# Performance work log

Measured on AMD Instinct MI355X. Metric: run time of the kernel, lower is better.

## Reference

```python
import jax, jax.numpy as jnp
import numpy as np


def setup_inputs() -> dict:
    key = jax.random.key(0)
    ks = jax.random.split(key, 18)
    B, T, L, C = 16, 512, 50, 7
    H = 512
    s = 0.05
    inp = {
        "phone_data": jax.random.normal(ks[0], (B, T, L, C), jnp.float32),
        "h0": jax.random.normal(ks[1], (B, H), jnp.float32),
        "conv1_w": jax.random.normal(ks[2], (128, 7, 11), jnp.float32) * s,
        "conv1_b": jax.random.normal(ks[3], (128,), jnp.float32) * s,
        "conv2_w": jax.random.normal(ks[4], (256, 128, 9), jnp.float32) * s,
        "conv2_b": jax.random.normal(ks[5], (256,), jnp.float32) * s,
        "fc1_w": jax.random.normal(ks[6], (1024, 1536), jnp.float32) * s,
        "fc1_b": jax.random.normal(ks[7], (1024,), jnp.float32) * s,
        "fc2_w": jax.random.normal(ks[8], (512, 1024), jnp.float32) * s,
        "fc2_b": jax.random.normal(ks[9], (512,), jnp.float32) * s,
        "gru_wih": jax.random.normal(ks[10], (3 * H, H), jnp.float32) * s,
        "gru_whh": jax.random.normal(ks[11], (3 * H, H), jnp.float32) * s,
        "gru_bih": jax.random.normal(ks[12], (3 * H,), jnp.float32) * s,
        "gru_bhh": jax.random.normal(ks[13], (3 * H,), jnp.float32) * s,
        "fc3_w": jax.random.normal(ks[14], (1, H), jnp.float32) * s,
        "fc3_b": jax.random.normal(ks[15], (1,), jnp.float32) * s,
    }
    return inp


def reference(phone_data, h0, conv1_w, conv1_b, conv2_w, conv2_b,
              fc1_w, fc1_b, fc2_w, fc2_b,
              gru_wih, gru_whh, gru_bih, gru_bhh, fc3_w, fc3_b):
    B, T, L, C = phone_data.shape
    N = B * T
    # ---- batched CNN + FC feature extractor (independent per frame) ----
    x = phone_data.reshape(N, L, C).transpose(0, 2, 1)  # [N, 7, 50]
    y = jax.lax.conv_general_dilated(
        x, conv1_w, (1,), 'VALID',
        dimension_numbers=('NCH', 'OIH', 'NCH')) + conv1_b[None, :, None]  # [N,128,40]
    y = y.reshape(N, 128, 20, 2).max(-1)  # maxpool k=2,s=2 -> [N,128,20]
    y = jax.lax.conv_general_dilated(
        y, conv2_w, (1,), 'VALID',
        dimension_numbers=('NCH', 'OIH', 'NCH')) + conv2_b[None, :, None]  # [N,256,12]
    y = y.reshape(N, 256, 6, 2).max(-1)  # [N,256,6]
    feat = y.reshape(N, 1536)            # Flatten(0): channel-major, matches torch
    feat = feat @ fc1_w.T + fc1_b        # [N,1024]
    feat = feat @ fc2_w.T + fc2_b        # [N,512]
    feat = feat.reshape(B, T, 512)

    # ---- sequential GRUCell recurrence (PyTorch GRUCell math) ----
    def cell(h, x_t):
        gi = x_t @ gru_wih.T + gru_bih   # [B, 3H]
        gh = h @ gru_whh.T + gru_bhh     # [B, 3H]
        ir, iz, in_ = jnp.split(gi, 3, axis=-1)
        hr, hz, hn = jnp.split(gh, 3, axis=-1)
        r = jax.nn.sigmoid(ir + hr)
        z = jax.nn.sigmoid(iz + hz)
        n = jnp.tanh(in_ + r * hn)
        h_new = (1 - z) * n + z * h
        # original code calls hx.detach() every step
        h_new = jax.lax.stop_gradient(h_new)
        return h_new, h_new

    _, hs = jax.lax.scan(cell, h0, feat.transpose(1, 0, 2))  # hs: [T,B,512]
    out = hs @ fc3_w.T + fc3_b  # [T,B,1]
    return out.transpose(1, 0, 2)  # [B,T,1]
```

## Files before the change

### kernel.cpp

```cpp
#include <hip/hip_runtime.h>
#include <hip/hip_bf16.h>
#include <math.h>
#include <stdint.h>

typedef __attribute__((ext_vector_type(8))) short short8;
typedef __attribute__((ext_vector_type(4))) float f32x4;
typedef __attribute__((ext_vector_type(4))) unsigned int uint4v;

#define T_ 512

__device__ __forceinline__ unsigned short bf16rn(float f) {
  union { float f; unsigned u; } x; x.f = f;
  unsigned r = x.u + 0x7FFF + ((x.u >> 16) & 1);
  return (unsigned short)(r >> 16);
}

__device__ __forceinline__ void gload16(const void* gsrc, void* ldst) {
  __builtin_amdgcn_global_load_lds(
      (const __attribute__((address_space(1))) unsigned int*)gsrc,
      (__attribute__((address_space(3))) unsigned int*)ldst, 16, 0, 0);
}

__device__ __forceinline__ void wg_barrier() {
  __builtin_amdgcn_sched_barrier(0);
  asm volatile("s_waitcnt lgkmcnt(0)" ::: "memory");
  __builtin_amdgcn_sched_barrier(0);
  __builtin_amdgcn_s_barrier();
  __builtin_amdgcn_sched_barrier(0);
}

__global__ __launch_bounds__(256) void conv1_kernel(
    const float* __restrict__ phone, const float* __restrict__ w1,
    const float* __restrict__ b1, ushort* __restrict__ out1b) {
  __shared__ float ws[128 * 77];
  __shared__ float bs[128];
  __shared__ float xs[8][7][52];
  const int tid = threadIdx.x;
  const int n0 = blockIdx.x * 8;
  for (int idx = tid; idx < 9856; idx += 256) ws[idx] = w1[idx];
  if (tid < 128) bs[tid] = b1[tid];
  for (int idx = tid; idx < 2800; idx += 256) {
    int fi = idx / 350, r = idx - fi * 350;
    int ll = r / 7, c = r - ll * 7;
    xs[fi][c][ll] = phone[(size_t)(n0 + fi) * 350 + r];
  }
  __syncthreads();

  const int o = tid >> 1, ph = tid & 1;
  const float* wo = ws + o * 77;
  const float bb = bs[o];
  for (int fi = 0; fi < 8; ++fi) {
    float acc0[10], acc1[10];
#pragma unroll
    for (int q = 0; q < 10; ++q) { acc0[q] = 0.f; acc1[q] = 0.f; }
    for (int i = 0; i < 7; ++i) {
      float wr[11];
#pragma unroll
      for (int k = 0; k < 11; ++k) wr[k] = wo[i * 11 + k];
#pragma unroll
      for (int q = 0; q < 10; ++q) {
        int p = ph * 10 + q;
        int base = 2 * p;
        float xv[12];
#pragma unroll
        for (int j = 0; j < 12; ++j) xv[j] = xs[fi][i][base + j];
        float s0 = 0.f, s1 = 0.f;
#pragma unroll
        for (int k = 0; k < 11; ++k) {
          s0 += xv[k] * wr[k];
          s1 += xv[k + 1] * wr[k];
        }
        acc0[q] += s0;
        acc1[q] += s1;
      }
    }
#pragma unroll
    for (int q = 0; q < 10; ++q) {
      int p = ph * 10 + q;
      out1b[((size_t)(n0 + fi) * 128 + o) * 20 + p] =
          bf16rn(fmaxf(acc0[q], acc1[q]) + bb);
    }
  }
}

__global__ __launch_bounds__(256) void f32_to_bf16_multi(
    const float* __restrict__ s0, ushort* __restrict__ d0,
    const float* __restrict__ s1, ushort* __restrict__ d1,
    const float* __restrict__ s2, ushort* __restrict__ d2,
    const float* __restrict__ s3, ushort* __restrict__ d3) {
  const int n0 = 73728, n1 = 393216, n2 = 131072, n3 = 196608;
  int i = blockIdx.x * 256 + threadIdx.x;
  const float* s; ushort* d; int off;
  if (i < n0) { s = s0; d = d0; off = i; }
  else if (i < n0 + n1) { s = s1; d = d1; off = i - n0; }
  else if (i < n0 + n1 + n2) { s = s2; d = d2; off = i - n0 - n1; }
  else if (i < n0 + n1 + n2 + n3) { s = s3; d = d3; off = i - n0 - n1 - n2; }
  else return;
  float4 v = ((const float4*)s)[off];
  ushort4 o;
  o.x = bf16rn(v.x); o.y = bf16rn(v.y); o.z = bf16rn(v.z); o.w = bf16rn(v.w);
  ((ushort4*)d)[off] = o;
}

__global__ __launch_bounds__(256) void stage_h0(
    const float* __restrict__ h0, unsigned long long* __restrict__ hxt) {
  const int tid = threadIdx.x;
#pragma unroll
  for (int k = 0; k < 16; ++k) {
    int idx = tid + k * 256;
    int g = idx >> 11, rem = idx & 2047;
    int s = rem >> 7, w_i = rem & 127;
    int b8 = (w_i >> 2) & 7, fqk = w_i >> 5, p2 = w_i & 3;
    int b = g * 8 + b8;
    int D = s * 32 + fqk * 8 + p2 * 2;
    float2 h2 = *(const float2*)(h0 + (size_t)b * 512 + D);
    unsigned pk = (unsigned)bf16rn(h2.x) | ((unsigned)bf16rn(h2.y) << 16);
    hxt[8192 + (size_t)g * 4096 + s * 128 + w_i] = (unsigned long long)pk;
  }
}

template <int AM, int EM>
__global__ __launch_bounds__(256) void gemm_bf16(
    const ushort* __restrict__ A, const ushort* __restrict__ W,
    const float* __restrict__ bias, void* __restrict__ Cout,
    int K, int lda, int ldc) {
  __shared__ ushort As[128 * 64];
  __shared__ ushort Bs[128 * 64];
  __shared__ ushort tbl[1152];
  const int tid = threadIdx.x;
  const int l = tid & 63, wv = tid >> 6;
  const int wr = wv >> 1, wc = wv & 1;
  const int fr = l & 15, fq = l >> 4;
  const int bm0 = blockIdx.x * 128, bn0 = blockIdx.y * 128;

  if (AM == 1) {
    for (int idx = tid; idx < 1152; idx += 256) {
      int i2 = idx / 9, kp = idx - i2 * 9;
      tbl[idx] = (ushort)(i2 * 20 + kp);
    }
    __syncthreads();
  }

  f32x4 acc[4][4];
#pragma unroll
  for (int mi = 0; mi < 4; ++mi)
#pragma unroll
    for (int ni = 0; ni < 4; ++ni) acc[mi][ni] = (f32x4)0.f;

  const int pr8 = l >> 3;
  const int pc = l & 7;
  const int nkt = K >> 6;
  for (int kt = 0; kt < nkt; ++kt) {
    const int k0 = kt << 6;
#pragma unroll
    for (int i = 0; i < 4; ++i) {
      int q = wv * 4 + i;
      int prow = q * 8 + pr8;
      int lc = pc ^ (prow & 7);
      gload16(W + (size_t)(bn0 + prow) * K + k0 + lc * 8, &Bs[q * 512]);
    }
    if (AM == 0) {
#pragma unroll
      for (int i = 0; i < 4; ++i) {
        int q = wv * 4 + i;
        int prow = q * 8 + pr8;
        int lc = pc ^ (prow & 7);
        gload16(A + (size_t)(bm0 + prow) * lda + k0 + lc * 8, &As[q * 512]);
      }
    } else {
#pragma unroll
      for (int q = 0; q < 16; ++q) {
        int idx = tid + q * 256;
        int row = idx >> 5, c0 = (idx & 31) * 2;
        int m = bm0 + row;
        int n = m / 12, pos = m - n * 12;
        int kk = k0 + c0;
        const ushort* an = A + (size_t)n * 2560 + pos;
        uint e0 = an[tbl[kk]];
        uint e1 = an[tbl[kk + 1]];
        *(uint*)&As[row * 64 + (((c0 >> 3) ^ (row & 7)) << 3) + (c0 & 7)] =
            e0 | (e1 << 16);
      }
    }
    __syncthreads();
#pragma unroll
    for (int ks = 0; ks < 2; ++ks) {
      short8 af[4], bfr[4];
#pragma unroll
      for (int mi = 0; mi < 4; ++mi) {
        int row = wr * 64 + mi * 16 + fr;
        af[mi] = *(const short8*)&As[row * 64 + (((ks * 4 + fq) ^ (row & 7)) << 3)];
      }
#pragma unroll
      for (int ni = 0; ni < 4; ++ni) {
        int row = wc * 64 + ni * 16 + fr;
        bfr[ni] = *(const short8*)&Bs[row * 64 + (((ks * 4 + fq) ^ (row & 7)) << 3)];
      }
#pragma unroll
      for (int mi = 0; mi < 4; ++mi)
#pragma unroll
        for (int ni = 0; ni < 4; ++ni)
          acc[mi][ni] = __builtin_amdgcn_mfma_f32_16x16x32_bf16(
              af[mi], bfr[ni], acc[mi][ni], 0, 0, 0);
    }
    __syncthreads();
  }

#pragma unroll
  for (int ni = 0; ni < 4; ++ni) {
    int col = bn0 + wc * 64 + ni * 16 + fr;
    float bv = bias[col];
#pragma unroll
    for (int mi = 0; mi < 4; ++mi) {
      int mbase = bm0 + wr * 64 + mi * 16 + fq * 4;
      if (EM == 0) {
        ushort* C = (ushort*)Cout;
#pragma unroll
        for (int j = 0; j < 4; ++j)
          C[(size_t)(mbase + j) * ldc + col] = bf16rn(acc[mi][ni][j] + bv);
      } else if (EM == 1) {
        ushort* C = (ushort*)Cout;
#pragma unroll
        for (int j = 0; j < 4; j += 2) {
          int m = mbase + j;
          int n = m / 12, pos = m - n * 12;
          float v = fmaxf(acc[mi][ni][j], acc[mi][ni][j + 1]) + bv;
          C[(size_t)n * 1536 + col * 6 + (pos >> 1)] = bf16rn(v);
        }
      } else {
        float* C = (float*)Cout;
#pragma unroll
        for (int j = 0; j < 4; ++j) {
          int m = mbase + j;
          int b = m >> 9, tt = m & 511;
          C[((size_t)tt * 16 + b) * 1536 + col] = acc[mi][ni][j] + bv;
        }
      }
    }
  }
}

__global__ __launch_bounds__(384) void gru_persistent(
    const float* __restrict__ h0, const float* __restrict__ gi,
    const float* __restrict__ whh, const float* __restrict__ bhh,
    float* __restrict__ hsbuf, unsigned long long* __restrict__ hxt) {
  __shared__ float gh_lds[12 * 256];
  __shared__ unsigned afl[16 * 64 * 4];
  const int tid = threadIdx.x;
  const int g = blockIdx.x & 7, wp = blockIdx.x >> 3;
  if (g >= 2) return;
  const int l = tid & 63, v = tid >> 6;
  const int fr = l & 15, fq = l >> 4;
  unsigned long long* hxl = hxt + (size_t)g * 4096;
  unsigned long long* hxm = hxt + 8192 + (size_t)g * 4096;

  const int b8 = tid >> 5, jp = tid & 31, jl = jp * 2;
  const bool gthr = (tid < 256);
  const int pt = tid - 256;

  int s_w = 0, w_w = 0;
  if (gthr) {
    s_w = wp * 2 + (jl >> 5);
    w_w = (((jl & 31) >> 3) * 8 + b8) * 4 + (jp & 3);
    *(volatile unsigned long long*)(hxl + s_w * 128 + w_w) = 0ull;
    *(volatile unsigned long long*)(hxl + 2048 + s_w * 128 + w_w) = 0ull;
  }

  const int t0 = 2 * v, t1 = 2 * v + 1;
  const int o0 = (t0 >> 2) * 512 + wp * 64 + (t0 & 3) * 16 + fr;
  const int o1 = (t1 >> 2) * 512 + wp * 64 + (t1 & 3) * 16 + fr;
  short8 bf0[16], bf1[16];
#pragma unroll
  for (int s = 0; s < 16; ++s) {
    const float* wp0 = whh + (size_t)o0 * 512 + s * 32 + fq * 8;
    const float* wp1 = whh + (size_t)o1 * 512 + s * 32 + fq * 8;
    float4 a0 = *(const float4*)wp0, a1 = *(const float4*)(wp0 + 4);
    float4 c0 = *(const float4*)wp1, c1 = *(const float4*)(wp1 + 4);
    short8 x, y;
    x[0] = (short)bf16rn(a0.x); x[1] = (short)bf16rn(a0.y);
    x[2] = (short)bf16rn(a0.z); x[3] = (short)bf16rn(a0.w);
    x[4] = (short)bf16rn(a1.x); x[5] = (short)bf16rn(a1.y);
    x[6] = (short)bf16rn(a1.z); x[7] = (short)bf16rn(a1.w);
    y[0] = (short)bf16rn(c0.x); y[1] = (short)bf16rn(c0.y);
    y[2] = (short)bf16rn(c0.z); y[3] = (short)bf16rn(c0.w);
    y[4] = (short)bf16rn(c1.x); y[5] = (short)bf16rn(c1.y);
    y[6] = (short)bf16rn(c1.z); y[7] = (short)bf16rn(c1.w);
    bf0[s] = x; bf1[s] = y;
  }
  const float bo0 = bhh[o0], bo1 = bhh[o1];

  const int bglob = g * 8 + b8;
  const int jglob = wp * 64 + jl;
  float hA = 0.f, hB = 0.f;
  float giC0 = 0.f, giC1 = 0.f, giC2 = 0.f, giC3 = 0.f, giC4 = 0.f, giC5 = 0.f;
  float giN0 = 0.f, giN1 = 0.f, giN2 = 0.f, giN3 = 0.f, giN4 = 0.f, giN5 = 0.f;
  if (gthr) {
    float2 h2 = *(const float2*)(h0 + (size_t)bglob * 512 + jglob);
    hA = h2.x; hB = h2.y;
    const float* g0 = gi + (size_t)bglob * 1536 + jglob;
    float2 r0 = *(const float2*)(g0);
    float2 r1 = *(const float2*)(g0 + 512);
    float2 r2 = *(const float2*)(g0 + 1024);
    giC0 = r0.x; giC3 = r0.y; giC1 = r1.x; giC4 = r1.y; giC2 = r2.x; giC5 = r2.y;
    const float* g1 = gi + (size_t)(16 + bglob) * 1536 + jglob;
    float2 s0 = *(const float2*)(g1);
    float2 s1 = *(const float2*)(g1 + 512);
    float2 s2 = *(const float2*)(g1 + 1024);
    giN0 = s0.x; giN3 = s0.y; giN1 = s1.x; giN4 = s1.y; giN2 = s2.x; giN5 = s2.y;
  }

  bool useMir = false;
  if (!gthr) {
    const int ps = pt >> 3;
    const int pw0 = (pt & 7) * 2;
    const unsigned long long* base = hxm + ps * 128;
    uint4v r[8];
    for (;;) {
#pragma unroll
      for (int m = 0; m < 8; ++m)
        asm volatile("global_load_dwordx4 %0, %1, off sc0 sc1"
                     : "=v"(r[m]) : "v"(base + pw0 + m * 16));
      asm volatile("s_waitcnt vmcnt(0)" ::: "memory");
      __builtin_amdgcn_sched_barrier(0);
      bool ok = true;
#pragma unroll
      for (int m = 0; m < 8; ++m)
        ok = ok & (r[m].y == 0u) & (r[m].w == 0u);
      if (ok) break;
    }
#pragma unroll
    for (int m = 0; m < 8; ++m) {
      int w_i = pw0 + m * 16;
      int lane = ((w_i >> 2) & 7) + 16 * (w_i >> 5);
      *(uint2*)&afl[(ps * 64 + lane) * 4 + (w_i & 3)] = make_uint2(r[m].x, r[m].z);
    }
  }
  wg_barrier();

  for (int t = 0; t < T_; ++t) {
    f32x4 e0 = (f32x4)0.f, q0 = (f32x4)0.f, e1 = (f32x4)0.f, q1 = (f32x4)0.f;
#pragma unroll
    for (int s = 0; s < 16; s += 2) {
      union { uint4v u; short8 s8; } ca, cb;
      ca.u = *(const uint4v*)&afl[((s + 0) * 64 + l) * 4];
      cb.u = *(const uint4v*)&afl[((s + 1) * 64 + l) * 4];
      e0 = __builtin_amdgcn_mfma_f32_16x16x32_bf16(ca.s8, bf0[s], e0, 0, 0, 0);
      q0 = __builtin_amdgcn_mfma_f32_16x16x32_bf16(cb.s8, bf0[s + 1], q0, 0, 0, 0);
      e1 = __builtin_amdgcn_mfma_f32_16x16x32_bf16(ca.s8, bf1[s], e1, 0, 0, 0);
      q1 = __builtin_amdgcn_mfma_f32_16x16x32_bf16(cb.s8, bf1[s + 1], q1, 0, 0, 0);
    }
#pragma unroll
    for (int j = 0; j < 4; ++j) {
      gh_lds[t0 * 256 + (fq * 4 + j) * 16 + fr] = e0[j] + q0[j] + bo0;
      gh_lds[t1 * 256 + (fq * 4 + j) * 16 + fr] = e1[j] + q1[j] + bo1;
    }
    wg_barrier();

    if (gthr) {
      const int hh = jl >> 4, c = jl & 15;
      float2 rr = *(const float2*)&gh_lds[(0 + hh) * 256 + b8 * 16 + c];
      float2 zz = *(const float2*)&gh_lds[(4 + hh) * 256 + b8 * 16 + c];
      float2 nn = *(const float2*)&gh_lds[(8 + hh) * 256 + b8 * 16 + c];
      float rgA = __builtin_amdgcn_rcpf(1.f + __expf(-(giC0 + rr.x)));
      float rgB = __builtin_amdgcn_rcpf(1.f + __expf(-(giC3 + rr.y)));
      float zgA = __builtin_amdgcn_rcpf(1.f + __expf(-(giC1 + zz.x)));
      float zgB = __builtin_amdgcn_rcpf(1.f + __expf(-(giC4 + zz.y)));
      float eA = __expf(2.f * (giC2 + rgA * nn.x));
      float eB = __expf(2.f * (giC5 + rgB * nn.y));
      float ngA = 1.f - 2.f * __builtin_amdgcn_rcpf(eA + 1.f);
      float ngB = 1.f - 2.f * __builtin_amdgcn_rcpf(eB + 1.f);
      hA = (1.f - zgA) * ngA + zgA * hA;
      hB = (1.f - zgB) * ngB + zgB * hB;
      if (t + 1 < T_) {
        unsigned pk = (unsigned)bf16rn(hA) | ((unsigned)bf16rn(hB) << 16);
        unsigned long long payload =
            (unsigned long long)pk | ((unsigned long long)(unsigned)(t + 1) << 32);
        const size_t woff = (size_t)((t + 1) & 1) * 2048 + s_w * 128 + w_w;
        *(volatile unsigned long long*)(hxl + woff) = payload;
        __hip_atomic_store(hxm + woff, payload, __ATOMIC_RELAXED,
                           __HIP_MEMORY_SCOPE_AGENT);
      }
      *(float2*)(hsbuf + ((size_t)t * 16 + bglob) * 512 + jglob) =
          make_float2(hA, hB);
      giC0 = giN0; giC1 = giN1; giC2 = giN2;
      giC3 = giN3; giC4 = giN4; giC5 = giN5;
      if (t + 2 < T_) {
        const float* gb = gi + ((size_t)(t + 2) * 16 + bglob) * 1536 + jglob;
        float2 r0 = *(const float2*)(gb);
        float2 r1 = *(const float2*)(gb + 512);
        float2 r2 = *(const float2*)(gb + 1024);
        giN0 = r0.x; giN3 = r0.y; giN1 = r1.x; giN4 = r1.y; giN2 = r2.x; giN5 = r2.y;
      }
    } else if (t + 1 < T_) {
      const int ps = pt >> 3;
      const int pw0 = (pt & 7) * 2;
      const unsigned tag = (unsigned)(t + 1);
      const size_t poff = (size_t)((t + 1) & 1) * 2048 + ps * 128;
      uint4v r[8];
      bool done = false;
      if (!useMir && t + 1 >= 9) {
        const unsigned long long* base = hxl + poff;
        int iters = 24;
        do {
#pragma unroll
          for (int m = 0; m < 8; ++m)
            asm volatile("global_load_dwordx4 %0, %1, off sc0"
                         : "=v"(r[m]) : "v"(base + pw0 + m * 16));
          asm volatile("s_waitcnt vmcnt(0)" ::: "memory");
          __builtin_amdgcn_sched_barrier(0);
          bool ok = true;
#pragma unroll
          for (int m = 0; m < 8; ++m)
            ok = ok & (r[m].y == tag) & (r[m].w == tag);
          done = ok;
        } while (!done && --iters);
        if (!done) useMir = true;
      }
      if (!done) {
        const unsigned long long* base = hxm + poff;
        for (;;) {
#pragma unroll
          for (int m = 0; m < 8; ++m)
            asm volatile("global_load_dwordx4 %0, %1, off sc0 sc1"
                         : "=v"(r[m]) : "v"(base + pw0 + m * 16));
          asm volatile("s_waitcnt vmcnt(0)" ::: "memory");
          __builtin_amdgcn_sched_barrier(0);
          bool ok = true;
#pragma unroll
          for (int m = 0; m < 8; ++m)
            ok = ok & (r[m].y == tag) & (r[m].w == tag);
          if (ok) break;
        }
      }
#pragma unroll
      for (int m = 0; m < 8; ++m) {
        int w_i = pw0 + m * 16;
        int lane = ((w_i >> 2) & 7) + 16 * (w_i >> 5);
        *(uint2*)&afl[(ps * 64 + lane) * 4 + (w_i & 3)] = make_uint2(r[m].x, r[m].z);
      }
    }
    wg_barrier();
  }
}

__global__ __launch_bounds__(256) void fc3_kernel(
    const float* __restrict__ hs, const float* __restrict__ w3,
    const float* __restrict__ b3, float* __restrict__ out) {
  __shared__ float w[512];
  const int tid = threadIdx.x;
  w[tid] = w3[tid];
  w[tid + 256] = w3[tid + 256];
  __syncthreads();
  const int gidx = blockIdx.x * 256 + tid;
  const int b = gidx >> 9, t = gidx & 511;
  const float4* hr = (const float4*)(hs + ((size_t)t * 16 + b) * 512);
  const float4* wr = (const float4*)w;
  float acc = 0.f;
#pragma unroll 8
  for (int kc = 0; kc < 128; ++kc) {
    float4 h = hr[kc], ww = wr[kc];
    acc += h.x * ww.x + h.y * ww.y + h.z * ww.z + h.w * ww.w;
  }
  out[gidx] = acc + b3[0];
}

extern "C" void kernel_launch(void* const* d_in, const int* in_sizes, int n_in,
                              void* d_out, int out_size, void* d_ws,
                              size_t ws_size, hipStream_t stream) {
  const float* phone = (const float*)d_in[0];
  const float* h0    = (const float*)d_in[1];
  const float* w1    = (const float*)d_in[2];
  const float* b1    = (const float*)d_in[3];
  const float* w2    = (const float*)d_in[4];
  const float* b2    = (const float*)d_in[5];
  const float* fc1w  = (const float*)d_in[6];
  const float* fc1b  = (const float*)d_in[7];
  const float* fc2w  = (const float*)d_in[8];
  const float* fc2b  = (const float*)d_in[9];
  const float* wih   = (const float*)d_in[10];
  const float* whh   = (const float*)d_in[11];
  const float* bih   = (const float*)d_in[12];
  const float* bhh   = (const float*)d_in[13];
  const float* w3    = (const float*)d_in[14];
  const float* b3    = (const float*)d_in[15];
  float* out = (float*)d_out;

  char* ws = (char*)d_ws;
  ushort* out1b = (ushort*)(ws + 0);
  ushort* feat2 = (ushort*)(ws + 41943040);
  ushort* feat3 = (ushort*)(ws + 67108864);
  ushort* feat4 = (ushort*)(ws + 83886080);
  float*  gibuf = (float*) (ws + 92274688);
  float*  hsbuf = (float*) (ws + 142606336);
  ushort* w2b   = (ushort*)(ws + 159383552);
  ushort* fc1wb = (ushort*)(ws + 159973376);
  ushort* fc2wb = (ushort*)(ws + 163119104);
  ushort* wihb  = (ushort*)(ws + 164167680);
  unsigned long long* hxt = (unsigned long long*)(ws + 67108864);

  f32_to_bf16_multi<<<3104, 256, 0, stream>>>(w2, w2b, fc1w, fc1wb,
                                              fc2w, fc2wb, wih, wihb);

  conv1_kernel<<<1024, 256, 0, stream>>>(phone, w1, b1, out1b);
  gemm_bf16<1, 1><<<dim3(768, 2), 256, 0, stream>>>(out1b, w2b, b2, feat2, 1152, 0, 0);
  gemm_bf16<0, 0><<<dim3(64, 8), 256, 0, stream>>>(feat2, fc1wb, fc1b, feat3, 1536, 1536, 1024);
  gemm_bf16<0, 0><<<dim3(64, 4), 256, 0, stream>>>(feat3, fc2wb, fc2b, feat4, 1024, 1024, 512);
  gemm_bf16<0, 2><<<dim3(64, 12), 256, 0, stream>>>(feat4, wihb, bih, gibuf, 512, 512, 1536);

  hipMemsetAsync(hxt, 0, 131072, stream);
  stage_h0<<<1, 256, 0, stream>>>(h0, hxt);
  gru_persistent<<<64, 384, 0, stream>>>(h0, gibuf, whh, bhh, hsbuf, hxt);

  fc3_kernel<<<32, 256, 0, stream>>>(hsbuf, w3, b3, out);
}
```

Baseline: 1.820 ms.

## Restructure GRU recurrence with double-buffered LDS and a single coherent exchange buffer

The persistent GRU kernel now launches only the 16 blocks that do work. It maps groups by blockIdx>>3, which spreads each batch group across XCDs. The separate local and mirror hidden-state buffers and the adaptive fallback between them are replaced by one buffer read with system-coherent loads. Four waves now compute three gate tiles each while the polling wave pre-polls the next step into a double-buffered LDS slot, so communication can overlap with the MFMA work. The aim is to shorten the per-step critical path. The cost is that the XCD-local L2 fast path is given up, so every step goes through slower cross-XCD coherence.

After: 1.985 ms. 9.1% more time.

```diff
diff --git a/kernel.cpp b/kernel.cpp
--- a/kernel.cpp
+++ b/kernel.cpp
@@ -115,7 +115,7 @@
     int D = s * 32 + fqk * 8 + p2 * 2;
     float2 h2 = *(const float2*)(h0 + (size_t)b * 512 + D);
     unsigned pk = (unsigned)bf16rn(h2.x) | ((unsigned)bf16rn(h2.y) << 16);
-    hxt[8192 + (size_t)g * 4096 + s * 128 + w_i] = (unsigned long long)pk;
+    hxt[(size_t)g * 4096 + s * 128 + w_i] = (unsigned long long)pk;
   }
 }
 
@@ -245,49 +245,50 @@
     const float* __restrict__ whh, const float* __restrict__ bhh,
     float* __restrict__ hsbuf, unsigned long long* __restrict__ hxt) {
   __shared__ float gh_lds[12 * 256];
-  __shared__ unsigned afl[16 * 64 * 4];
+  __shared__ unsigned afl[2][4096];
   const int tid = threadIdx.x;
-  const int g = blockIdx.x & 7, wp = blockIdx.x >> 3;
-  if (g >= 2) return;
+  const int g = blockIdx.x >> 3, wp = blockIdx.x & 7;
   const int l = tid & 63, v = tid >> 6;
   const int fr = l & 15, fq = l >> 4;
-  unsigned long long* hxl = hxt + (size_t)g * 4096;
-  unsigned long long* hxm = hxt + 8192 + (size_t)g * 4096;
+  unsigned long long* hxg = hxt + (size_t)g * 4096;
 
   const int b8 = tid >> 5, jp = tid & 31, jl = jp * 2;
   const bool gthr = (tid < 256);
   const int pt = tid - 256;
 
-  int s_w = 0, w_w = 0;
-  if (gthr) {
-    s_w = wp * 2 + (jl >> 5);
-    w_w = (((jl & 31) >> 3) * 8 + b8) * 4 + (jp & 3);
-    *(volatile unsigned long long*)(hxl + s_w * 128 + w_w) = 0ull;
-    *(volatile unsigned long long*)(hxl + 2048 + s_w * 128 + w_w) = 0ull;
-  }
-
-  const int t0 = 2 * v, t1 = 2 * v + 1;
-  const int o0 = (t0 >> 2) * 512 + wp * 64 + (t0 & 3) * 16 + fr;
-  const int o1 = (t1 >> 2) * 512 + wp * 64 + (t1 & 3) * 16 + fr;
-  short8 bf0[16], bf1[16];
-#pragma unroll
-  for (int s = 0; s < 16; ++s) {
-    const float* wp0 = whh + (size_t)o0 * 512 + s * 32 + fq * 8;
-    const float* wp1 = whh + (size_t)o1 * 512 + s * 32 + fq * 8;
-    float4 a0 = *(const float4*)wp0, a1 = *(const float4*)(wp0 + 4);
-    float4 c0 = *(const float4*)wp1, c1 = *(const float4*)(wp1 + 4);
-    short8 x, y;
-    x[0] = (short)bf16rn(a0.x); x[1] = (short)bf16rn(a0.y);
-    x[2] = (short)bf16rn(a0.z); x[3] = (short)bf16rn(a0.w);
-    x[4] = (short)bf16rn(a1.x); x[5] = (short)bf16rn(a1.y);
-    x[6] = (short)bf16rn(a1.z); x[7] = (short)bf16rn(a1.w);
-    y[0] = (short)bf16rn(c0.x); y[1] = (short)bf16rn(c0.y);
-    y[2] = (short)bf16rn(c0.z); y[3] = (short)bf16rn(c0.w);
-    y[4] = (short)bf16rn(c1.x); y[5] = (short)bf16rn(c1.y);
-    y[6] = (short)bf16rn(c1.z); y[7] = (short)bf16rn(c1.w);
-    bf0[s] = x; bf1[s] = y;
-  }
-  const float bo0 = bhh[o0], bo1 = bhh[o1];
+  short8 bfA[16], bfB[16], bfC[16];
+  float boA = 0.f, boB = 0.f, boC = 0.f;
+  int tA = 0, tB = 0, tC = 0;
+  if (v < 4) {
+    tA = 3 * v; tB = 3 * v + 1; tC = 3 * v + 2;
+    const int oA = (tA >> 2) * 512 + wp * 64 + (tA & 3) * 16 + fr;
+    const int oB = (tB >> 2) * 512 + wp * 64 + (tB & 3) * 16 + fr;
+    const int oC = (tC >> 2) * 512 + wp * 64 + (tC & 3) * 16 + fr;
+#pragma unroll
+    for (int s = 0; s < 16; ++s) {
+      const float* pA = whh + (size_t)oA * 512 + s * 32 + fq * 8;
+      const float* pB = whh + (size_t)oB * 512 + s * 32 + fq * 8;
+      const float* pC = whh + (size_t)oC * 512 + s * 32 + fq * 8;
+      float4 a0 = *(const float4*)pA, a1 = *(const float4*)(pA + 4);
+      float4 b0 = *(const float4*)pB, b1 = *(const float4*)(pB + 4);
+      float4 c0 = *(const float4*)pC, c1 = *(const float4*)(pC + 4);
+      short8 x, y, z;
+      x[0] = (short)bf16rn(a0.x); x[1] = (short)bf16rn(a0.y);
+      x[2] = (short)bf16rn(a0.z); x[3] = (short)bf16rn(a0.w);
+      x[4] = (short)bf16rn(a1.x); x[5] = (short)bf16rn(a1.y);
+      x[6] = (short)bf16rn(a1.z); x[7] = (short)bf16rn(a1.w);
+      y[0] = (short)bf16rn(b0.x); y[1] = (short)bf16rn(b0.y);
+      y[2] = (short)bf16rn(b0.z); y[3] = (short)bf16rn(b0.w);
+      y[4] = (short)bf16rn(b1.x); y[5] = (short)bf16rn(b1.y);
+      y[6] = (short)bf16rn(b1.z); y[7] = (short)bf16rn(b1.w);
+      z[0] = (short)bf16rn(c0.x); z[1] = (short)bf16rn(c0.y);
+      z[2] = (short)bf16rn(c0.z); z[3] = (short)bf16rn(c0.w);
+      z[4] = (short)bf16rn(c1.x); z[5] = (short)bf16rn(c1.y);
+      z[6] = (short)bf16rn(c1.z); z[7] = (short)bf16rn(c1.w);
+      bfA[s] = x; bfB[s] = y; bfC[s] = z;
+    }
+    boA = bhh[oA]; boB = bhh[oB]; boC = bhh[oC];
+  }
 
   const int bglob = g * 8 + b8;
   const int jglob = wp * 64 + jl;
@@ -309,11 +310,10 @@
     giN0 = s0.x; giN3 = s0.y; giN1 = s1.x; giN4 = s1.y; giN2 = s2.x; giN5 = s2.y;
   }
 
-  bool useMir = false;
   if (!gthr) {
     const int ps = pt >> 3;
     const int pw0 = (pt & 7) * 2;
-    const unsigned long long* base = hxm + ps * 128;
+    const unsigned long long* base = hxg + ps * 128;
     uint4v r[8];
     for (;;) {
 #pragma unroll
@@ -332,31 +332,31 @@
     for (int m = 0; m < 8; ++m) {
       int w_i = pw0 + m * 16;
       int lane = ((w_i >> 2) & 7) + 16 * (w_i >> 5);
-      *(uint2*)&afl[(ps * 64 + lane) * 4 + (w_i & 3)] = make_uint2(r[m].x, r[m].z);
+      *(uint2*)&afl[0][(ps * 64 + lane) * 4 + (w_i & 3)] =
+          make_uint2(r[m].x, r[m].z);
     }
   }
   wg_barrier();
 
   for (int t = 0; t < T_; ++t) {
-    f32x4 e0 = (f32x4)0.f, q0 = (f32x4)0.f, e1 = (f32x4)0.f, q1 = (f32x4)0.f;
-#pragma unroll
-    for (int s = 0; s < 16; s += 2) {
-      union { uint4v u; short8 s8; } ca, cb;
-      ca.u = *(const uint4v*)&afl[((s + 0) * 64 + l) * 4];
-      cb.u = *(const uint4v*)&afl[((s + 1) * 64 + l) * 4];
-      e0 = __builtin_amdgcn_mfma_f32_16x16x32_bf16(ca.s8, bf0[s], e0, 0, 0, 0);
-      q0 = __builtin_amdgcn_mfma_f32_16x16x32_bf16(cb.s8, bf0[s + 1], q0, 0, 0, 0);
-      e1 = __builtin_amdgcn_mfma_f32_16x16x32_bf16(ca.s8, bf1[s], e1, 0, 0, 0);
-      q1 = __builtin_amdgcn_mfma_f32_16x16x32_bf16(cb.s8, bf1[s + 1], q1, 0, 0, 0);
-    }
-#pragma unroll
-    for (int j = 0; j < 4; ++j) {
-      gh_lds[t0 * 256 + (fq * 4 + j) * 16 + fr] = e0[j] + q0[j] + bo0;
-      gh_lds[t1 * 256 + (fq * 4 + j) * 16 + fr] = e1[j] + q1[j] + bo1;
-    }
-    wg_barrier();
-
-    if (gthr) {
+    const int par = t & 1;
+    if (v < 4) {
+      f32x4 aA = (f32x4)0.f, aB = (f32x4)0.f, aC = (f32x4)0.f;
+#pragma unroll
+      for (int s = 0; s < 16; ++s) {
+        union { uint4v u; short8 s8; } ca;
+        ca.u = *(const uint4v*)&afl[par][(s * 64 + l) * 4];
+        aA = __builtin_amdgcn_mfma_f32_16x16x32_bf16(ca.s8, bfA[s], aA, 0, 0, 0);
+        aB = __builtin_amdgcn_mfma_f32_16x16x32_bf16(ca.s8, bfB[s], aB, 0, 0, 0);
+        aC = __builtin_amdgcn_mfma_f32_16x16x32_bf16(ca.s8, bfC[s], aC, 0, 0, 0);
+      }
+#pragma unroll
+      for (int j = 0; j < 4; ++j) {
+        gh_lds[tA * 256 + (fq * 4 + j) * 16 + fr] = aA[j] + boA;
+        gh_lds[tB * 256 + (fq * 4 + j) * 16 + fr] = aB[j] + boB;
+        gh_lds[tC * 256 + (fq * 4 + j) * 16 + fr] = aC[j] + boC;
+      }
+      wg_barrier();
       const int hh = jl >> 4, c = jl & 15;
       float2 rr = *(const float2*)&gh_lds[(0 + hh) * 256 + b8 * 16 + c];
       float2 zz = *(const float2*)&gh_lds[(4 + hh) * 256 + b8 * 16 + c];
@@ -375,10 +375,10 @@
         unsigned pk = (unsigned)bf16rn(hA) | ((unsigned)bf16rn(hB) << 16);
         unsigned long long payload =
             (unsigned long long)pk | ((unsigned long long)(unsigned)(t + 1) << 32);
-        const size_t woff = (size_t)((t + 1) & 1) * 2048 + s_w * 128 + w_w;
-        *(volatile unsigned long long*)(hxl + woff) = payload;
-        __hip_atomic_store(hxm + woff, payload, __ATOMIC_RELAXED,
-                           __HIP_MEMORY_SCOPE_AGENT);
+        int s = wp * 2 + (jl >> 5);
+        int w_i = (((jl & 31) >> 3) * 8 + b8) * 4 + (jp & 3);
+        __hip_atomic_store(hxg + ((t + 1) & 1) * 2048 + s * 128 + w_i, payload,
+                           __ATOMIC_RELAXED, __HIP_MEMORY_SCOPE_AGENT);
       }
       *(float2*)(hsbuf + ((size_t)t * 16 + bglob) * 512 + jglob) =
           make_float2(hA, hB);
@@ -391,33 +391,40 @@
         float2 r2 = *(const float2*)(gb + 1024);
         giN0 = r0.x; giN3 = r0.y; giN1 = r1.x; giN4 = r1.y; giN2 = r2.x; giN5 = r2.y;
       }
-    } else if (t + 1 < T_) {
+      wg_barrier();
+    } else {
       const int ps = pt >> 3;
       const int pw0 = (pt & 7) * 2;
       const unsigned tag = (unsigned)(t + 1);
-      const size_t poff = (size_t)((t + 1) & 1) * 2048 + ps * 128;
+      const int npar = (t + 1) & 1;
       uint4v r[8];
-      bool done = false;
-      if (!useMir && t + 1 >= 9) {
-        const unsigned long long* base = hxl + poff;
-        int iters = 24;
-        do {
-#pragma unroll
-          for (int m = 0; m < 8; ++m)
-            asm volatile("global_load_dwordx4 %0, %1, off sc0"
-                         : "=v"(r[m]) : "v"(base + pw0 + m * 16));
-          asm volatile("s_waitcnt vmcnt(0)" ::: "memory");
-          __builtin_amdgcn_sched_barrier(0);
-          bool ok = true;
-#pragma unroll
-          for (int m = 0; m < 8; ++m)
-            ok = ok & (r[m].y == tag) & (r[m].w == tag);
-          done = ok;
-        } while (!done && --iters);
-        if (!done) useMir = true;
-      }
+      bool done = (t + 1 >= T_);
+      for (int it = 0; it < 3 && !done; ++it) {
+        const unsigned long long* base = hxg + (size_t)npar * 2048 + ps * 128;
+#pragma unroll
+        for (int m = 0; m < 8; ++m)
+          asm volatile("global_load_dwordx4 %0, %1, off sc0 sc1"
+                       : "=v"(r[m]) : "v"(base + pw0 + m * 16));
+        asm volatile("s_waitcnt vmcnt(0)" ::: "memory");
+        __builtin_amdgcn_sched_barrier(0);
+        bool ok = true;
+#pragma unroll
+        for (int m = 0; m < 8; ++m)
+          ok = ok & (r[m].y == tag) & (r[m].w == tag);
+        done = ok;
+      }
+      if (done && t + 1 < T_) {
+#pragma unroll
+        for (int m = 0; m < 8; ++m) {
+          int w_i = pw0 + m * 16;
+          int lane = ((w_i >> 2) & 7) + 16 * (w_i >> 5);
+          *(uint2*)&afl[npar][(ps * 64 + lane) * 4 + (w_i & 3)] =
+              make_uint2(r[m].x, r[m].z);
+        }
+      }
+      wg_barrier();
       if (!done) {
-        const unsigned long long* base = hxm + poff;
+        const unsigned long long* base = hxg + (size_t)npar * 2048 + ps * 128;
         for (;;) {
 #pragma unroll
           for (int m = 0; m < 8; ++m)
@@ -431,15 +438,16 @@
             ok = ok & (r[m].y == tag) & (r[m].w == tag);
           if (ok) break;
         }
-      }
-#pragma unroll
-      for (int m = 0; m < 8; ++m) {
-        int w_i = pw0 + m * 16;
-        int lane = ((w_i >> 2) & 7) + 16 * (w_i >> 5);
-        *(uint2*)&afl[(ps * 64 + lane) * 4 + (w_i & 3)] = make_uint2(r[m].x, r[m].z);
-      }
-    }
-    wg_barrier();
+#pragma unroll
+        for (int m = 0; m < 8; ++m) {
+          int w_i = pw0 + m * 16;
+          int lane = ((w_i >> 2) & 7) + 16 * (w_i >> 5);
+          *(uint2*)&afl[npar][(ps * 64 + lane) * 4 + (w_i & 3)] =
+              make_uint2(r[m].x, r[m].z);
+        }
+      }
+      wg_barrier();
+    }
   }
 }
 
@@ -507,9 +515,9 @@
   gemm_bf16<0, 0><<<dim3(64, 4), 256, 0, stream>>>(feat3, fc2wb, fc2b, feat4, 1024, 1024, 512);
   gemm_bf16<0, 2><<<dim3(64, 12), 256, 0, stream>>>(feat4, wihb, bih, gibuf, 512, 512, 1536);
 
-  hipMemsetAsync(hxt, 0, 131072, stream);
+  hipMemsetAsync(hxt, 0, 65536, stream);
   stage_h0<<<1, 256, 0, stream>>>(h0, hxt);
-  gru_persistent<<<64, 384, 0, stream>>>(h0, gibuf, whh, bhh, hsbuf, hxt);
+  gru_persistent<<<16, 384, 0, stream>>>(h0, gibuf, whh, bhh, hsbuf, hxt);
 
   fc3_kernel<<<32, 256, 0, stream>>>(hsbuf, w3, b3, out);
 }
```
